# Kernel optimization log

Measured on AMD Instinct MI355X. Metric: run time of the kernel, lower is better.

The kernel has to match this reference:

```python
import jax, jax.numpy as jnp
import numpy as np
import math

N_HEAD = 8
D_MODEL = 512
HEAD_SIZE = D_MODEL // N_HEAD
VOCAB = 16384
BLOCK = 512
LN_EPS = 1e-5


def sinusoidal_pe(max_len, dim):
    pos = np.arange(max_len)[:, None].astype(np.float32)
    div = np.exp(np.arange(0, dim, 2).astype(np.float32) * (-math.log(10000.0) / dim))
    pe = np.zeros((max_len, dim), dtype=np.float32)
    pe[:, 0::2] = np.sin(pos * div)
    pe[:, 1::2] = np.cos(pos * div)
    return jnp.asarray(pe)  # (max_len, hs)


def setup_inputs() -> dict:
    key = jax.random.key(0)
    ks = jax.random.split(key, 6)
    b, t = 4, BLOCK
    return {
        "x": jax.random.normal(ks[0], (b, t, 1), dtype=jnp.float32),
        "embedding": jax.random.normal(ks[1], (N_HEAD, VOCAB, HEAD_SIZE), dtype=jnp.float32),
        "enc_w": jax.random.normal(ks[2], (D_MODEL, 1), dtype=jnp.float32) * 0.05,
        "enc_b": jax.random.normal(ks[3], (D_MODEL,), dtype=jnp.float32) * 0.05,
        "ln_w": jnp.ones((HEAD_SIZE,), dtype=jnp.float32),
        "ln_b": jnp.zeros((HEAD_SIZE,), dtype=jnp.float32),
        "dec_w": jax.random.normal(ks[4], (1, D_MODEL), dtype=jnp.float32) * 0.05,
        "dec_b": jax.random.normal(ks[5], (1,), dtype=jnp.float32) * 0.05,
    }


def reference(x, embedding, enc_w, enc_b, ln_w, ln_b, dec_w, dec_b):
    b, t, _ = x.shape
    # encoder: Linear(input_dim -> d_model)
    h = x @ enc_w.T + enc_b                              # (b, t, d_model)
    h = h.reshape(b, t, N_HEAD, HEAD_SIZE).transpose(0, 2, 1, 3)  # (b, nh, t, hs)
    # sinusoidal positional encoding over time, added to head dim
    h = h + sinusoidal_pe(BLOCK, HEAD_SIZE)[:t]
    # LayerNorm over hs
    mu = h.mean(-1, keepdims=True)
    var = ((h - mu) ** 2).mean(-1, keepdims=True)
    h = (h - mu) * jax.lax.rsqrt(var + LN_EPS) * ln_w + ln_b
    # attention over shared per-head codebook
    scores = jnp.einsum('bnth,nvh->bntv', h, embedding) / math.sqrt(D_MODEL)
    probs = jax.nn.softmax(scores, axis=-1)              # (b, nh, t, vocab)
    quant = jnp.einsum('bntv,nvh->bnth', probs, embedding)
    quant = quant.transpose(0, 2, 1, 3).reshape(b, t, D_MODEL)
    # decoder: Linear(d_model -> output_dim)
    return quant @ dec_w.T + dec_b                       # (b, t, 1)
```

## Files before the change

kernel.cpp:

```cpp
#include <hip/hip_runtime.h>
#include <hip/hip_bf16.h>
#include <math.h>

#define NH 8
#define HS 64
#define VOCAB 16384
#define QPH 2048
#define QSCALE (0.04419417382415922f * 1.4426950408889634f)

typedef __attribute__((ext_vector_type(8))) short bf16x8;
typedef __attribute__((ext_vector_type(4))) float f32x4;

static __device__ __forceinline__ unsigned short f2bf(float f) {
    __hip_bfloat16 h = __float2bfloat16(f);
    unsigned short u;
    __builtin_memcpy(&u, &h, 2);
    return u;
}

static __device__ __forceinline__ float fexp2(float x) {
#if __has_builtin(__builtin_amdgcn_exp2f)
    return __builtin_amdgcn_exp2f(x);
#else
    return __expf(x * 0.6931471805599453f);
#endif
}

__global__ void prep(const float* __restrict__ x, const float* __restrict__ emb,
                     const float* __restrict__ enc_w, const float* __restrict__ enc_b,
                     const float* __restrict__ ln_w, const float* __restrict__ ln_b,
                     const float* __restrict__ dec_w,
                     unsigned short* __restrict__ qbf, unsigned short* __restrict__ ebf,
                     float* __restrict__ g) {
    if (blockIdx.x < 8192) {
        int i4  = blockIdx.x * 256 + threadIdx.x;
        int row = i4 >> 4;
        int c   = i4 & 15;
        int n   = row >> 14;
        f32x4 v = ((const f32x4*)emb)[i4];
        ushort4 u = make_ushort4(f2bf(v.x), f2bf(v.y), f2bf(v.z), f2bf(v.w));
        ((ushort4*)ebf)[i4] = u;
        const float* dw = dec_w + n * 64 + c * 4;
        float p = v.x * dw[0] + v.y * dw[1] + v.z * dw[2] + v.w * dw[3];
        p += __shfl_xor(p, 1); p += __shfl_xor(p, 2);
        p += __shfl_xor(p, 4); p += __shfl_xor(p, 8);
        if (c == 0) g[row] = p;
    } else {
        int row  = (blockIdx.x - 8192) * 4 + (threadIdx.x >> 6);
        int h    = threadIdx.x & 63;
        int n = row >> 11;
        int q = row & 2047;
        int t = q & 511;
        float xv = x[q];
        int d = n * 64 + h;
        float h2  = (float)(h & ~1);
        float div = __expf(h2 * (-9.210340371976184f / 64.0f));
        float ang = (float)t * div;
        float pe  = (h & 1) ? __cosf(ang) : __sinf(ang);
        float v = xv * enc_w[d] + enc_b[d] + pe;
        float s = v;
        #pragma unroll
        for (int off = 1; off < 64; off <<= 1) s += __shfl_xor(s, off);
        float mu = s * (1.0f / 64.0f);
        float dd = v - mu;
        float s2 = dd * dd;
        #pragma unroll
        for (int off = 1; off < 64; off <<= 1) s2 += __shfl_xor(s2, off);
        float var = s2 * (1.0f / 64.0f);
        float y = dd * rsqrtf(var + 1e-5f) * ln_w[h] + ln_b[h];
        qbf[row * 64 + h] = f2bf(y * QSCALE);
    }
}

__global__ void __launch_bounds__(256, 4)
attn(const unsigned short* __restrict__ qbf, const unsigned short* __restrict__ ebf,
     const float* __restrict__ g, float* __restrict__ part) {
    int tid  = threadIdx.x;
    int w    = tid >> 6;
    int lane = tid & 63;
    int quad = lane >> 4;
    int l15  = lane & 15;
    int hv     = blockIdx.x & 127;
    int head   = hv & 7;
    int vslice = hv >> 3;
    int qchunk = blockIdx.x >> 7;
    int qbase  = (qchunk * 4 + w) * 64;

    const short* qp = (const short*)qbf + (size_t)(head * QPH + qbase) * HS;
    bf16x8 qf[4][2];
    #pragma unroll
    for (int qt = 0; qt < 4; ++qt) {
        const short* qrow = qp + (qt * 16 + l15) * HS + quad * 8;
        qf[qt][0] = *(const bf16x8*)(qrow);
        qf[qt][1] = *(const bf16x8*)(qrow + 32);
    }

    const short* ep = (const short*)ebf + ((size_t)head * VOCAB + vslice * 1024) * HS;
    const float* gp = g + head * VOCAB + vslice * 1024;

    float num[4] = {0.f, 0.f, 0.f, 0.f};
    float den[4] = {0.f, 0.f, 0.f, 0.f};
    const f32x4 z = {0.f, 0.f, 0.f, 0.f};

    for (int it = 0; it < 32; ++it) {
        int vb = it * 32;
        const short* e0 = ep + (size_t)(vb + l15) * HS + quad * 8;
        const short* e1 = ep + (size_t)(vb + 16 + l15) * HS + quad * 8;
        bf16x8 a00 = *(const bf16x8*)(e0);
        bf16x8 a01 = *(const bf16x8*)(e0 + 32);
        bf16x8 a10 = *(const bf16x8*)(e1);
        bf16x8 a11 = *(const bf16x8*)(e1 + 32);
        f32x4 gv0 = *(const f32x4*)(gp + vb + quad * 4);
        f32x4 gv1 = *(const f32x4*)(gp + vb + 16 + quad * 4);
        #pragma unroll
        for (int qt = 0; qt < 4; ++qt) {
            f32x4 acc0 = __builtin_amdgcn_mfma_f32_16x16x32_bf16(a00, qf[qt][0], z, 0, 0, 0);
            acc0       = __builtin_amdgcn_mfma_f32_16x16x32_bf16(a01, qf[qt][1], acc0, 0, 0, 0);
            f32x4 acc1 = __builtin_amdgcn_mfma_f32_16x16x32_bf16(a10, qf[qt][0], z, 0, 0, 0);
            acc1       = __builtin_amdgcn_mfma_f32_16x16x32_bf16(a11, qf[qt][1], acc1, 0, 0, 0);
            #pragma unroll
            for (int r = 0; r < 4; ++r) {
                float p0 = fexp2(acc0[r]);
                float p1 = fexp2(acc1[r]);
                den[qt] += p0 + p1;
                num[qt] += p0 * gv0[r] + p1 * gv1[r];
            }
        }
    }

    #pragma unroll
    for (int qt = 0; qt < 4; ++qt) {
        num[qt] += __shfl_xor(num[qt], 16); num[qt] += __shfl_xor(num[qt], 32);
        den[qt] += __shfl_xor(den[qt], 16); den[qt] += __shfl_xor(den[qt], 32);
    }
    int qg = qbase + quad * 16 + l15;
    float nv = num[quad];
    float dv = den[quad];
    float* pp = part + (size_t)(head * QPH + qg) * 2;
    atomicAdd(pp,     nv);
    atomicAdd(pp + 1, dv);
}

__global__ void fin(const float* __restrict__ part, const float* __restrict__ dec_b,
                    float* __restrict__ out) {
    int q = blockIdx.x * 256 + threadIdx.x;
    float s = dec_b[0];
    #pragma unroll
    for (int n = 0; n < NH; ++n) {
        float nv = part[(size_t)(n * QPH + q) * 2];
        float dv = part[(size_t)(n * QPH + q) * 2 + 1];
        s += nv / dv;
    }
    out[q] = s;
}

extern "C" void kernel_launch(void* const* d_in, const int* in_sizes, int n_in,
                              void* d_out, int out_size, void* d_ws, size_t ws_size,
                              hipStream_t stream) {
    const float* x     = (const float*)d_in[0];
    const float* emb   = (const float*)d_in[1];
    const float* enc_w = (const float*)d_in[2];
    const float* enc_b = (const float*)d_in[3];
    const float* ln_w  = (const float*)d_in[4];
    const float* ln_b  = (const float*)d_in[5];
    const float* dec_w = (const float*)d_in[6];
    const float* dec_b = (const float*)d_in[7];
    float* out = (float*)d_out;

    char* ws = (char*)d_ws;
    unsigned short* qbf  = (unsigned short*)(ws);
    unsigned short* ebf  = (unsigned short*)(ws + 2097152);
    float*          g    = (float*)(ws + 2097152 + 16777216);
    float*          part = (float*)(ws + 2097152 + 16777216 + 524288);
    size_t part_bytes = (size_t)NH * QPH * 2 * sizeof(float);

    hipMemsetAsync(part, 0, part_bytes, stream);
    hipLaunchKernelGGL(prep, dim3(12288), dim3(256), 0, stream,
                       x, emb, enc_w, enc_b, ln_w, ln_b, dec_w, qbf, ebf, g);
    hipLaunchKernelGGL(attn, dim3(1024), dim3(256), 0, stream, qbf, ebf, g, part);
    hipLaunchKernelGGL(fin,  dim3(8),    dim3(256), 0, stream, part, dec_b, out);
}
```

Measured before the change: 170.2 us.

## Prefetch codebook tiles one iteration ahead and replace atomics with per-slice partials

The attention loop now loads the next iteration's embedding and g values into registers before running the current MFMAs, a software-pipelined prefetch meant to hide global load latency. The atomicAdd accumulation of numerator and denominator is replaced by plain float2 stores into a per-vocab-slice partial buffer. The final kernel then sums the 16 slices, which also removes the memset launch. The cost is more registers in the hot loop, which could hurt occupancy, plus a larger partial buffer for the finalize step to read. The prefetch wraps around on the last iteration and issues one redundant load.

```diff
diff --git a/kernel.cpp b/kernel.cpp
--- a/kernel.cpp
+++ b/kernel.cpp
@@ -74,15 +74,14 @@
 
 __global__ void __launch_bounds__(256, 4)
 attn(const unsigned short* __restrict__ qbf, const unsigned short* __restrict__ ebf,
-     const float* __restrict__ g, float* __restrict__ part) {
+     const float* __restrict__ g, float2* __restrict__ part) {
     int tid  = threadIdx.x;
     int w    = tid >> 6;
     int lane = tid & 63;
     int quad = lane >> 4;
     int l15  = lane & 15;
-    int hv     = blockIdx.x & 127;
-    int head   = hv & 7;
-    int vslice = hv >> 3;
+    int head   = blockIdx.x & 7;
+    int vslice = (blockIdx.x >> 3) & 15;
     int qchunk = blockIdx.x >> 7;
     int qbase  = (qchunk * 4 + w) * 64;
 
@@ -102,16 +101,26 @@
     float den[4] = {0.f, 0.f, 0.f, 0.f};
     const f32x4 z = {0.f, 0.f, 0.f, 0.f};
 
+    const short* e0 = ep + (size_t)l15 * HS + quad * 8;
+    const short* e1 = ep + (size_t)(16 + l15) * HS + quad * 8;
+    bf16x8 a00 = *(const bf16x8*)(e0);
+    bf16x8 a01 = *(const bf16x8*)(e0 + 32);
+    bf16x8 a10 = *(const bf16x8*)(e1);
+    bf16x8 a11 = *(const bf16x8*)(e1 + 32);
+    f32x4 gv0 = *(const f32x4*)(gp + quad * 4);
+    f32x4 gv1 = *(const f32x4*)(gp + 16 + quad * 4);
+
     for (int it = 0; it < 32; ++it) {
-        int vb = it * 32;
-        const short* e0 = ep + (size_t)(vb + l15) * HS + quad * 8;
-        const short* e1 = ep + (size_t)(vb + 16 + l15) * HS + quad * 8;
-        bf16x8 a00 = *(const bf16x8*)(e0);
-        bf16x8 a01 = *(const bf16x8*)(e0 + 32);
-        bf16x8 a10 = *(const bf16x8*)(e1);
-        bf16x8 a11 = *(const bf16x8*)(e1 + 32);
-        f32x4 gv0 = *(const f32x4*)(gp + vb + quad * 4);
-        f32x4 gv1 = *(const f32x4*)(gp + vb + 16 + quad * 4);
+        int vb2 = ((it + 1) & 31) * 32;
+        const short* n0 = ep + (size_t)(vb2 + l15) * HS + quad * 8;
+        const short* n1 = ep + (size_t)(vb2 + 16 + l15) * HS + quad * 8;
+        bf16x8 b00 = *(const bf16x8*)(n0);
+        bf16x8 b01 = *(const bf16x8*)(n0 + 32);
+        bf16x8 b10 = *(const bf16x8*)(n1);
+        bf16x8 b11 = *(const bf16x8*)(n1 + 32);
+        f32x4 ngv0 = *(const f32x4*)(gp + vb2 + quad * 4);
+        f32x4 ngv1 = *(const f32x4*)(gp + vb2 + 16 + quad * 4);
+
         #pragma unroll
         for (int qt = 0; qt < 4; ++qt) {
             f32x4 acc0 = __builtin_amdgcn_mfma_f32_16x16x32_bf16(a00, qf[qt][0], z, 0, 0, 0);
@@ -126,6 +135,8 @@
                 num[qt] += p0 * gv0[r] + p1 * gv1[r];
             }
         }
+        a00 = b00; a01 = b01; a10 = b10; a11 = b11;
+        gv0 = ngv0; gv1 = ngv1;
     }
 
     #pragma unroll
@@ -134,21 +145,21 @@
         den[qt] += __shfl_xor(den[qt], 16); den[qt] += __shfl_xor(den[qt], 32);
     }
     int qg = qbase + quad * 16 + l15;
-    float nv = num[quad];
-    float dv = den[quad];
-    float* pp = part + (size_t)(head * QPH + qg) * 2;
-    atomicAdd(pp,     nv);
-    atomicAdd(pp + 1, dv);
+    part[((size_t)vslice * NH + head) * QPH + qg] = make_float2(num[quad], den[quad]);
 }
 
-__global__ void fin(const float* __restrict__ part, const float* __restrict__ dec_b,
+__global__ void fin(const float2* __restrict__ part, const float* __restrict__ dec_b,
                     float* __restrict__ out) {
     int q = blockIdx.x * 256 + threadIdx.x;
     float s = dec_b[0];
     #pragma unroll
     for (int n = 0; n < NH; ++n) {
-        float nv = part[(size_t)(n * QPH + q) * 2];
-        float dv = part[(size_t)(n * QPH + q) * 2 + 1];
+        float nv = 0.f, dv = 0.f;
+        #pragma unroll
+        for (int sl = 0; sl < 16; ++sl) {
+            float2 nd = part[((size_t)sl * NH + n) * QPH + q];
+            nv += nd.x; dv += nd.y;
+        }
         s += nv / dv;
     }
     out[q] = s;
@@ -171,10 +182,8 @@
     unsigned short* qbf  = (unsigned short*)(ws);
     unsigned short* ebf  = (unsigned short*)(ws + 2097152);
     float*          g    = (float*)(ws + 2097152 + 16777216);
-    float*          part = (float*)(ws + 2097152 + 16777216 + 524288);
-    size_t part_bytes = (size_t)NH * QPH * 2 * sizeof(float);
+    float2*         part = (float2*)(ws + 2097152 + 16777216 + 524288);
 
-    hipMemsetAsync(part, 0, part_bytes, stream);
     hipLaunchKernelGGL(prep, dim3(12288), dim3(256), 0, stream,
                        x, emb, enc_w, enc_b, ln_w, ln_b, dec_w, qbf, ebf, g);
     hipLaunchKernelGGL(attn, dim3(1024), dim3(256), 0, stream, qbf, ebf, g, part);
```

New measurement: 170.2 us. No clear change (-0.0%).
